# Performance work log

Hardware: AMD Instinct MI355X
Metric: run time of the kernel (lower is better)

The kernel has to match this reference:

```python
import jax, jax.numpy as jnp
import numpy as np


def setup_inputs() -> dict:
    key = jax.random.key(0)
    ks = jax.random.split(key, 8)
    B, S, H = 4, 2048, 1024
    heads = 16
    lim = 1.0 / np.sqrt(H)  # nn.Linear default init range
    x = jax.random.normal(ks[0], (B, S, H), dtype=jnp.float32)
    atten_mask = jnp.zeros((B, 1, S, 1), dtype=jnp.float32)  # 1.0 marks padded positions
    Wq = jax.random.uniform(ks[1], (H, H), jnp.float32, -lim, lim)
    bq = jax.random.uniform(ks[2], (H,), jnp.float32, -lim, lim)
    Wk = jax.random.uniform(ks[3], (H, H), jnp.float32, -lim, lim)
    bk = jax.random.uniform(ks[4], (H,), jnp.float32, -lim, lim)
    Wv = jax.random.uniform(ks[5], (H, H), jnp.float32, -lim, lim)
    bv = jax.random.uniform(ks[6], (H,), jnp.float32, -lim, lim)
    return {"x": x, "Wq": Wq, "bq": bq, "Wk": Wk, "bk": bk, "Wv": Wv, "bv": bv,
            "atten_mask": atten_mask, "attention_head_num": 16}


def reference(x, Wq, bq, Wk, bk, Wv, bv, atten_mask, attention_head_num):
    B, S, H = x.shape
    h = attention_head_num
    d = H // h
    # QKV projections (torch Linear: x @ W.T + b)
    q = (x @ Wq.T + bq).reshape(B, S, h, d).transpose(0, 2, 1, 3)  # [B,h,S,d]
    k = (x @ Wk.T + bk).reshape(B, S, h, d).transpose(0, 2, 1, 3)
    v = (x @ Wv.T + bv).reshape(B, S, h, d).transpose(0, 2, 1, 3)
    # combined padding + look-ahead mask: True -> masked
    causal = jnp.triu(jnp.ones((S, S), dtype=atten_mask.dtype), 1)  # [S,S]
    mask = (atten_mask + causal) >= 1.0  # [B,1 or h,S,S] broadcast
    mask = jnp.broadcast_to(mask, (B, h, S, S))
    scale = 1.0 / jnp.sqrt(jnp.asarray(d, dtype=jnp.float32))
    scores = jnp.einsum('bhqd,bhkd->bhqk', q, k) * scale
    scores = jnp.where(mask, jnp.float32(-1e9), scores)
    att = jax.nn.softmax(scores, axis=-1)
    out = jnp.einsum('bhqk,bhkd->bhqd', att, v)  # [B,h,S,d]
    return out.transpose(0, 2, 1, 3).reshape(B, S, H)
```

## Files before the change

kernel.cpp:

```cpp
#include <hip/hip_runtime.h>
#include <hip/hip_bf16.h>
#include <stdint.h>

typedef short v8s __attribute__((ext_vector_type(8)));
typedef float v4f __attribute__((ext_vector_type(4)));
typedef unsigned long long u64;
typedef unsigned short u16;
typedef unsigned int u32;
typedef u64 v2u __attribute__((ext_vector_type(2)));

__device__ __forceinline__ u16 f2bf(float f) {
    unsigned u = __builtin_bit_cast(unsigned, f);
    u += 0x7FFFu + ((u >> 16) & 1u);
    return (u16)(u >> 16);
}

__device__ __forceinline__ u32 cvt_pk_bf16(float lo, float hi) {
    u32 r;
    asm("v_cvt_pk_bf16_f32 %0, %1, %2" : "=v"(r) : "v"(lo), "v"(hi));
    return r;
}

__device__ __forceinline__ float ex2(float x) {
    float r;
    asm("v_exp_f32 %0, %1" : "=v"(r) : "v"(x));
    return r;
}

__device__ __forceinline__ void gload_lds16(const void* g, const void* lds) {
    __builtin_amdgcn_global_load_lds(
        (const __attribute__((address_space(1))) unsigned int*)(unsigned long long)g,
        (__attribute__((address_space(3))) unsigned int*)(unsigned int)(unsigned long long)lds,
        16, 0, 0);
}

__global__ __launch_bounds__(256) void cvt_all(const float* __restrict__ x,
                                               const float* __restrict__ wq,
                                               const float* __restrict__ wk,
                                               const float* __restrict__ wv,
                                               u16* __restrict__ xb, u16* __restrict__ wqb,
                                               u16* __restrict__ wkb, u16* __restrict__ wvb) {
    int i = blockIdx.x * 256 + threadIdx.x;
    const float* in;
    u16* out;
    if (i < 2097152)      { in = x;  out = xb; }
    else if (i < 2359296) { in = wq; out = wqb; i -= 2097152; }
    else if (i < 2621440) { in = wk; out = wkb; i -= 2359296; }
    else                  { in = wv; out = wvb; i -= 2621440; }
    float4 v = ((const float4*)in)[i];
    ((ushort4*)out)[i] = make_ushort4(f2bf(v.x), f2bf(v.y), f2bf(v.z), f2bf(v.w));
}

__global__ __launch_bounds__(256, 4)
void qkv_gemm_all(const u16* __restrict__ X,
                  const u16* __restrict__ Wq, const u16* __restrict__ Wk, const u16* __restrict__ Wv,
                  const float* __restrict__ bq, const float* __restrict__ bk, const float* __restrict__ bv,
                  u16* __restrict__ Qg, u16* __restrict__ Kg, u16* __restrict__ VTg) {
    __shared__ __align__(16) char smem[34816];
    char* ldsA = smem;
    char* ldsB = smem + 16384;
    u16*  ldsE = (u16*)smem;

    const int l = (blockIdx.x & 7) * 192 + (blockIdx.x >> 3);
    const int mode = l >> 9;
    const int bx = l & 511;
    const u16* W = (mode == 0) ? Wq : (mode == 1) ? Wk : Wv;
    const float* bias = (mode == 0) ? bq : (mode == 1) ? bk : bv;
    u16* Out = (mode == 0) ? Qg : (mode == 1) ? Kg : VTg;

    const int t = threadIdx.x;
    const int lane = t & 63, wave = t >> 6;
    const int lhi = lane >> 4, llo = lane & 15;
    const int wm = wave >> 1, wn = wave & 1;
    const int m0 = (bx >> 3) * 128;
    const int n0 = (bx & 7) * 128;

    const int srow = (t * 16) >> 7;
    const int ssc = ((t * 16) >> 4) & 7;
    v4f acc[4][4] = {};

    for (int k0 = 0; k0 < 1024; k0 += 64) {
        #pragma unroll
        for (int i = 0; i < 4; ++i) {
            int row = i * 32 + srow;
            int c = ssc ^ (row & 7);
            const char* wbaseA = ldsA + (i * 256 + wave * 64) * 16;
            const char* wbaseB = ldsB + (i * 256 + wave * 64) * 16;
            gload_lds16(X + (m0 + row) * 1024 + k0 + c * 8, wbaseA);
            gload_lds16(W + (n0 + row) * 1024 + k0 + c * 8, wbaseB);
        }
        __syncthreads();
        __builtin_amdgcn_s_setprio(1);
        #pragma unroll
        for (int s = 0; s < 2; ++s) {
            v8s af[4], bf[4];
            #pragma unroll
            for (int i = 0; i < 4; ++i) {
                int r = wm * 64 + i * 16 + llo;
                af[i] = *(const v8s*)(ldsA + r * 128 + (((lhi + 4 * s) ^ (r & 7)) << 4));
            }
            #pragma unroll
            for (int j = 0; j < 4; ++j) {
                int r = wn * 64 + j * 16 + llo;
                bf[j] = *(const v8s*)(ldsB + r * 128 + (((lhi + 4 * s) ^ (r & 7)) << 4));
            }
            #pragma unroll
            for (int i = 0; i < 4; ++i)
                #pragma unroll
                for (int j = 0; j < 4; ++j)
                    acc[i][j] = __builtin_amdgcn_mfma_f32_16x16x32_bf16(af[i], bf[j], acc[i][j], 0, 0, 0);
        }
        __builtin_amdgcn_s_setprio(0);
        __syncthreads();
    }

    float bv_[4];
    #pragma unroll
    for (int j = 0; j < 4; ++j) bv_[j] = bias[n0 + wn * 64 + j * 16 + llo];
    const float scl = (mode == 0) ? 0.18033688011112042f : 1.0f;

    #pragma unroll
    for (int i = 0; i < 4; ++i) {
        #pragma unroll
        for (int j = 0; j < 4; ++j) {
            #pragma unroll
            for (int r = 0; r < 4; ++r) {
                int ml = wm * 64 + i * 16 + lhi * 4 + r;
                int nl = wn * 64 + j * 16 + llo;
                float v = (acc[i][j][r] + bv_[j]) * scl;
                u16 hh = f2bf(v);
                if (mode == 2) ldsE[nl * 136 + ml] = hh;
                else           ldsE[ml * 136 + nl] = hh;
            }
        }
    }
    __syncthreads();

    const int row = t >> 1, half = t & 1;
    if (mode == 2) {
        int n = n0 + row, hh = n >> 6, dd = n & 63;
        int b = m0 >> 11, sbase = (m0 & 2047) + half * 64;
        u16* dst = Out + ((b * 16 + hh) * 64 + dd) * 2048 + sbase;
        #pragma unroll
        for (int j = 0; j < 8; ++j)
            *(v8s*)(dst + j * 8) = *(const v8s*)&ldsE[row * 136 + half * 64 + j * 8];
    } else {
        int m = m0 + row, b = m >> 11, s = m & 2047;
        int hh = (n0 + half * 64) >> 6;
        u16* dst = Out + ((b * 16 + hh) * 2048 + s) * 64;
        #pragma unroll
        for (int j = 0; j < 8; ++j)
            *(v8s*)(dst + j * 8) = *(const v8s*)&ldsE[row * 136 + half * 64 + j * 8];
    }
}

__global__ __launch_bounds__(256, 6)
void flash_attn(const u16* __restrict__ Qg, const u16* __restrict__ Kg,
                const u16* __restrict__ VTg, const float* __restrict__ am,
                float* __restrict__ out) {
    __shared__ __align__(16) char smem[25088];
    char* ldsK = smem;
    char* ldsV = smem + 8192;
    char* ldsP = smem + 16384 + (threadIdx.x >> 6) * 2176;

    const int t = threadIdx.x;
    const int lane = t & 63, wave = t >> 6;
    const int lhi = lane >> 4, llo = lane & 15;
    const int bh = blockIdx.x;
    const int qi = 31 - blockIdx.y;
    const int b = bh >> 4, h = bh & 15;
    const int qw = qi * 64 + wave * 16;
    const int q = qw + llo;

    v8s qf[2];
    #pragma unroll
    for (int s = 0; s < 2; ++s)
        qf[s] = *(const v8s*)(Qg + (bh * 2048 + q) * 64 + lhi * 8 + 32 * s);

    v8s ones;
    #pragma unroll
    for (int j = 0; j < 8; ++j) ones[j] = (short)0x3F80;

    const float rowpen = am[b * 2048 + q];

    const int srow = (t * 16) >> 7, ssc = ((t * 16) >> 4) & 7;
    const int sc1 = ssc ^ (srow & 7), sc2 = ssc ^ ((srow + 32) & 7);
    #define STAGE(kj2) do {                                                        \
        const int kv0_ = (kj2) * 64;                                               \
        const char* wbK = ldsK + (wave * 64) * 16;                                 \
        const char* wbV = ldsV + (wave * 64) * 16;                                 \
        gload_lds16(Kg + (bh * 2048 + kv0_ + srow) * 64 + sc1 * 8, wbK);           \
        gload_lds16(VTg + (bh * 64 + srow) * 2048 + kv0_ + sc1 * 8, wbV);          \
        gload_lds16(Kg + (bh * 2048 + kv0_ + srow + 32) * 64 + sc2 * 8, wbK + 4096); \
        gload_lds16(VTg + (bh * 64 + srow + 32) * 2048 + kv0_ + sc2 * 8, wbV + 4096); \
    } while (0)

    float mrow = -1e30f;
    v4f lsum_acc = {};
    v4f o_acc[4] = {};

    for (int kj = 0; kj <= qi; ++kj) {
        STAGE(kj);
        __syncthreads();
        const int kv0 = kj * 64;

        const int nt4 = (kj == qi) ? (wave + 1) : 4;
        v4f sacc[4] = {};
        __builtin_amdgcn_s_setprio(1);
        #pragma unroll
        for (int tt = 0; tt < 4; ++tt) {
            if (tt < nt4) {
                #pragma unroll
                for (int s = 0; s < 2; ++s) {
                    int row = tt * 16 + llo;
                    int c = lhi + 4 * s;
                    v8s kb = *(const v8s*)(ldsK + row * 128 + ((c ^ (row & 7)) << 4));
                    sacc[tt] = __builtin_amdgcn_mfma_f32_16x16x32_bf16(kb, qf[s], sacc[tt], 0, 0, 0);
                }
            }
        }
        __builtin_amdgcn_s_setprio(0);

        if (kj == qi) {
            #pragma unroll
            for (int tt = 0; tt < 4; ++tt)
                #pragma unroll
                for (int r = 0; r < 4; ++r) {
                    int kvg = kv0 + tt * 16 + lhi * 4 + r;
                    if (kvg > q) sacc[tt][r] = -1e30f;
                }
        }
        if (rowpen >= 1.0f) {
            #pragma unroll
            for (int tt = 0; tt < 4; ++tt)
                #pragma unroll
                for (int r = 0; r < 4; ++r) sacc[tt][r] = -1e30f;
        }

        float m0_ = fmaxf(fmaxf(sacc[0][0], sacc[0][1]), sacc[0][2]);
        float m1_ = fmaxf(fmaxf(sacc[0][3], sacc[1][0]), sacc[1][1]);
        float m2_ = fmaxf(fmaxf(sacc[1][2], sacc[1][3]), sacc[2][0]);
        float m3_ = fmaxf(fmaxf(sacc[2][1], sacc[2][2]), sacc[2][3]);
        float m4_ = fmaxf(fmaxf(sacc[3][0], sacc[3][1]), fmaxf(sacc[3][2], sacc[3][3]));
        float lmx = fmaxf(fmaxf(fmaxf(m0_, m1_), fmaxf(m2_, m3_)), m4_);

        if (__any(lmx > mrow + 8.0f)) {
            float mx = fmaxf(lmx, __shfl_xor(lmx, 16));
            mx = fmaxf(mx, __shfl_xor(mx, 32));
            const float mn = fmaxf(mrow, mx);
            const float sc_o = ex2(mrow - mn);
            mrow = mn;
            #pragma unroll
            for (int r = 0; r < 4; ++r) lsum_acc[r] *= sc_o;
            #pragma unroll
            for (int dt = 0; dt < 4; ++dt)
                #pragma unroll
                for (int r = 0; r < 4; ++r) o_acc[dt][r] *= sc_o;
        }

        #pragma unroll
        for (int tt = 0; tt < 4; ++tt) {
            float p0 = ex2(sacc[tt][0] - mrow);
            float p1 = ex2(sacc[tt][1] - mrow);
            float p2 = ex2(sacc[tt][2] - mrow);
            float p3 = ex2(sacc[tt][3] - mrow);
            u32 w0 = cvt_pk_bf16(p0, p1);
            u32 w1 = cvt_pk_bf16(p2, p3);
            *(u64*)(ldsP + llo * 136 + tt * 32 + lhi * 8) = (u64)w0 | ((u64)w1 << 32);
        }

        __builtin_amdgcn_s_setprio(1);
        #pragma unroll
        for (int s = 0; s < 2; ++s) {
            u64 plo = *(const u64*)(ldsP + llo * 136 + lhi * 16 + s * 64);
            u64 phi = *(const u64*)(ldsP + llo * 136 + lhi * 16 + s * 64 + 8);
            v2u tmp; tmp.x = plo; tmp.y = phi;
            v8s pb = __builtin_bit_cast(v8s, tmp);
            lsum_acc = __builtin_amdgcn_mfma_f32_16x16x32_bf16(ones, pb, lsum_acc, 0, 0, 0);
            #pragma unroll
            for (int dt = 0; dt < 4; ++dt) {
                int vrow = dt * 16 + llo;
                v8s vb = *(const v8s*)(ldsV + vrow * 128 + (((lhi + 4 * s) ^ (vrow & 7)) << 4));
                o_acc[dt] = __builtin_amdgcn_mfma_f32_16x16x32_bf16(vb, pb, o_acc[dt], 0, 0, 0);
            }
        }
        __builtin_amdgcn_s_setprio(0);
        __syncthreads();
    }

    const float inv = 1.0f / lsum_acc[0];
    float* dst = out + (size_t)(b * 2048 + q) * 1024 + h * 64 + lhi * 4;
    #pragma unroll
    for (int dt = 0; dt < 4; ++dt) {
        float4 o;
        o.x = o_acc[dt][0] * inv;
        o.y = o_acc[dt][1] * inv;
        o.z = o_acc[dt][2] * inv;
        o.w = o_acc[dt][3] * inv;
        *(float4*)(dst + dt * 16) = o;
    }
}

extern "C" void kernel_launch(void* const* d_in, const int* in_sizes, int n_in,
                              void* d_out, int out_size, void* d_ws, size_t ws_size,
                              hipStream_t stream) {
    const float* x  = (const float*)d_in[0];
    const float* Wq = (const float*)d_in[1];
    const float* bq = (const float*)d_in[2];
    const float* Wk = (const float*)d_in[3];
    const float* bk = (const float*)d_in[4];
    const float* Wv = (const float*)d_in[5];
    const float* bv = (const float*)d_in[6];
    const float* amask = (const float*)d_in[7];
    float* out = (float*)d_out;

    char* ws = (char*)d_ws;
    u16* xb  = (u16*)(ws);
    u16* Wqb = (u16*)(ws + 16777216);
    u16* Wkb = (u16*)(ws + 16777216 + 2097152);
    u16* Wvb = (u16*)(ws + 16777216 + 2 * 2097152);
    u16* Qg  = (u16*)(ws + 23068672);
    u16* Kg  = (u16*)(ws + 39845888);
    u16* VTg = (u16*)(ws + 56623104);

    cvt_all<<<11264, 256, 0, stream>>>(x, Wq, Wk, Wv, xb, Wqb, Wkb, Wvb);
    qkv_gemm_all<<<1536, 256, 0, stream>>>(xb, Wqb, Wkb, Wvb, bq, bk, bv, Qg, Kg, VTg);
    flash_attn<<<dim3(64, 32), 256, 0, stream>>>(Qg, Kg, VTg, amask, out);
}
```

Baseline: 148.7 us.

## Double-buffer LDS tiles in QKV GEMM with prefetch two stages ahead

Turns the QKV projection GEMM's single-buffered K loop into a two-stage LDS ping-pong. The next tile's global-to-LDS loads are issued while the current tile feeds the MFMAs, and explicit vmcnt waits plus raw barriers replace __syncthreads. This doubles LDS per block to 64KB and lowers the occupancy hint from 4 to 2 blocks per CU, trading latency hiding across waves for in-block overlap.

```diff
diff --git a/kernel.cpp b/kernel.cpp
--- a/kernel.cpp
+++ b/kernel.cpp
@@ -51,14 +51,14 @@
     ((ushort4*)out)[i] = make_ushort4(f2bf(v.x), f2bf(v.y), f2bf(v.z), f2bf(v.w));
 }
 
-__global__ __launch_bounds__(256, 4)
+__global__ __launch_bounds__(256, 2)
 void qkv_gemm_all(const u16* __restrict__ X,
                   const u16* __restrict__ Wq, const u16* __restrict__ Wk, const u16* __restrict__ Wv,
                   const float* __restrict__ bq, const float* __restrict__ bk, const float* __restrict__ bv,
                   u16* __restrict__ Qg, u16* __restrict__ Kg, u16* __restrict__ VTg) {
-    __shared__ __align__(16) char smem[34816];
+    __shared__ __align__(16) char smem[65536];
     char* ldsA = smem;
-    char* ldsB = smem + 16384;
+    char* ldsB = smem + 32768;
     u16*  ldsE = (u16*)smem;
 
     const int l = (blockIdx.x & 7) * 192 + (blockIdx.x >> 3);
@@ -79,17 +79,31 @@
     const int ssc = ((t * 16) >> 4) & 7;
     v4f acc[4][4] = {};
 
-    for (int k0 = 0; k0 < 1024; k0 += 64) {
-        #pragma unroll
-        for (int i = 0; i < 4; ++i) {
-            int row = i * 32 + srow;
-            int c = ssc ^ (row & 7);
-            const char* wbaseA = ldsA + (i * 256 + wave * 64) * 16;
-            const char* wbaseB = ldsB + (i * 256 + wave * 64) * 16;
-            gload_lds16(X + (m0 + row) * 1024 + k0 + c * 8, wbaseA);
-            gload_lds16(W + (n0 + row) * 1024 + k0 + c * 8, wbaseB);
-        }
-        __syncthreads();
+    #define GSTAGE(kt) do {                                                          \
+        const int k0_ = (kt) * 64;                                                   \
+        char* dA = ldsA + ((kt) & 1) * 16384;                                        \
+        char* dB = ldsB + ((kt) & 1) * 16384;                                        \
+        _Pragma("unroll")                                                            \
+        for (int i_ = 0; i_ < 4; ++i_) {                                             \
+            int row = i_ * 32 + srow;                                                \
+            int c = ssc ^ (row & 7);                     \
+            gload_lds16(X + (m0 + row) * 1024 + k0_ + c * 8,                         \
+                        dA + (i_ * 256 + wave * 64) * 16);                           \
+            gload_lds16(W + (n0 + row) * 1024 + k0_ + c * 8,                         \
+                        dB + (i_ * 256 + wave * 64) * 16);                           \
+        }                                                                            \
+    } while (0)
+
+    GSTAGE(0);
+    GSTAGE(1);
+
+    for (int kt = 0; kt < 16; ++kt) {
+        if (kt < 15) asm volatile("s_waitcnt vmcnt(8)" ::: "memory");
+        else         asm volatile("s_waitcnt vmcnt(0)" ::: "memory");
+        __builtin_amdgcn_s_barrier();
+
+        const char* cA = ldsA + (kt & 1) * 16384;
+        const char* cB = ldsB + (kt & 1) * 16384;
         __builtin_amdgcn_s_setprio(1);
         #pragma unroll
         for (int s = 0; s < 2; ++s) {
@@ -97,12 +111,12 @@
             #pragma unroll
             for (int i = 0; i < 4; ++i) {
                 int r = wm * 64 + i * 16 + llo;
-                af[i] = *(const v8s*)(ldsA + r * 128 + (((lhi + 4 * s) ^ (r & 7)) << 4));
+                af[i] = *(const v8s*)(cA + r * 128 + (((lhi + 4 * s) ^ (r & 7)) << 4));
             }
             #pragma unroll
             for (int j = 0; j < 4; ++j) {
                 int r = wn * 64 + j * 16 + llo;
-                bf[j] = *(const v8s*)(ldsB + r * 128 + (((lhi + 4 * s) ^ (r & 7)) << 4));
+                bf[j] = *(const v8s*)(cB + r * 128 + (((lhi + 4 * s) ^ (r & 7)) << 4));
             }
             #pragma unroll
             for (int i = 0; i < 4; ++i)
@@ -111,7 +125,8 @@
                     acc[i][j] = __builtin_amdgcn_mfma_f32_16x16x32_bf16(af[i], bf[j], acc[i][j], 0, 0, 0);
         }
         __builtin_amdgcn_s_setprio(0);
-        __syncthreads();
+        __builtin_amdgcn_s_barrier();
+        if (kt + 2 < 16) GSTAGE(kt + 2);
     }
 
     float bv_[4];
```

New measurement: 149.4 us. No clear change (+0.4%).

## Widen QKV GEMM block tile to 128x256 to raise operand reuse

Applied to the files above, without the earlier changes.

The QKV projection GEMM now uses 128x256 output tiles per block (each wave computes 64x128), halving the grid to 768 blocks and doubling per-block LDS for the B operand. The epilogue writes the two 128-column halves through LDS in two passes. This lowers global and LDS traffic per FLOP by reusing each A fragment across more MFMAs, at the cost of more accumulator registers, lower occupancy (launch bounds 2) and fewer blocks to spread over CUs.

```diff
diff --git a/kernel.cpp b/kernel.cpp
--- a/kernel.cpp
+++ b/kernel.cpp
@@ -51,19 +51,19 @@
     ((ushort4*)out)[i] = make_ushort4(f2bf(v.x), f2bf(v.y), f2bf(v.z), f2bf(v.w));
 }
 
-__global__ __launch_bounds__(256, 4)
+__global__ __launch_bounds__(256, 2)
 void qkv_gemm_all(const u16* __restrict__ X,
                   const u16* __restrict__ Wq, const u16* __restrict__ Wk, const u16* __restrict__ Wv,
                   const float* __restrict__ bq, const float* __restrict__ bk, const float* __restrict__ bv,
                   u16* __restrict__ Qg, u16* __restrict__ Kg, u16* __restrict__ VTg) {
-    __shared__ __align__(16) char smem[34816];
+    __shared__ __align__(16) char smem[49152];
     char* ldsA = smem;
     char* ldsB = smem + 16384;
     u16*  ldsE = (u16*)smem;
 
-    const int l = (blockIdx.x & 7) * 192 + (blockIdx.x >> 3);
-    const int mode = l >> 9;
-    const int bx = l & 511;
+    const int l = (blockIdx.x & 7) * 96 + (blockIdx.x >> 3);
+    const int mode = l >> 8;
+    const int bx = l & 255;
     const u16* W = (mode == 0) ? Wq : (mode == 1) ? Wk : Wv;
     const float* bias = (mode == 0) ? bq : (mode == 1) ? bk : bv;
     u16* Out = (mode == 0) ? Qg : (mode == 1) ? Kg : VTg;
@@ -72,85 +72,93 @@
     const int lane = t & 63, wave = t >> 6;
     const int lhi = lane >> 4, llo = lane & 15;
     const int wm = wave >> 1, wn = wave & 1;
-    const int m0 = (bx >> 3) * 128;
-    const int n0 = (bx & 7) * 128;
-
-    const int srow = (t * 16) >> 7;
-    const int ssc = ((t * 16) >> 4) & 7;
-    v4f acc[4][4] = {};
+    const int m0 = (bx >> 2) * 128;
+    const int n0 = (bx & 3) * 256;
+
+    const int srow = t >> 3;
+    const int ssc = t & 7;
+    v4f acc[4][8] = {};
 
     for (int k0 = 0; k0 < 1024; k0 += 64) {
         #pragma unroll
         for (int i = 0; i < 4; ++i) {
             int row = i * 32 + srow;
             int c = ssc ^ (row & 7);
-            const char* wbaseA = ldsA + (i * 256 + wave * 64) * 16;
-            const char* wbaseB = ldsB + (i * 256 + wave * 64) * 16;
-            gload_lds16(X + (m0 + row) * 1024 + k0 + c * 8, wbaseA);
-            gload_lds16(W + (n0 + row) * 1024 + k0 + c * 8, wbaseB);
+            gload_lds16(X + (m0 + row) * 1024 + k0 + c * 8,
+                        ldsA + (i * 256 + wave * 64) * 16);
+        }
+        #pragma unroll
+        for (int i = 0; i < 8; ++i) {
+            int row = i * 32 + srow;
+            int c = ssc ^ (row & 7);
+            gload_lds16(W + (n0 + row) * 1024 + k0 + c * 8,
+                        ldsB + (i * 256 + wave * 64) * 16);
         }
         __syncthreads();
         __builtin_amdgcn_s_setprio(1);
         #pragma unroll
         for (int s = 0; s < 2; ++s) {
-            v8s af[4], bf[4];
+            v8s af[4], bf[8];
             #pragma unroll
             for (int i = 0; i < 4; ++i) {
                 int r = wm * 64 + i * 16 + llo;
                 af[i] = *(const v8s*)(ldsA + r * 128 + (((lhi + 4 * s) ^ (r & 7)) << 4));
             }
             #pragma unroll
-            for (int j = 0; j < 4; ++j) {
-                int r = wn * 64 + j * 16 + llo;
+            for (int j = 0; j < 8; ++j) {
+                int r = wn * 128 + j * 16 + llo;
                 bf[j] = *(const v8s*)(ldsB + r * 128 + (((lhi + 4 * s) ^ (r & 7)) << 4));
             }
             #pragma unroll
             for (int i = 0; i < 4; ++i)
                 #pragma unroll
-                for (int j = 0; j < 4; ++j)
+                for (int j = 0; j < 8; ++j)
                     acc[i][j] = __builtin_amdgcn_mfma_f32_16x16x32_bf16(af[i], bf[j], acc[i][j], 0, 0, 0);
         }
         __builtin_amdgcn_s_setprio(0);
         __syncthreads();
     }
 
-    float bv_[4];
-    #pragma unroll
-    for (int j = 0; j < 4; ++j) bv_[j] = bias[n0 + wn * 64 + j * 16 + llo];
+    float bv_[8];
+    #pragma unroll
+    for (int j = 0; j < 8; ++j) bv_[j] = bias[n0 + wn * 128 + j * 16 + llo];
     const float scl = (mode == 0) ? 0.18033688011112042f : 1.0f;
 
     #pragma unroll
-    for (int i = 0; i < 4; ++i) {
-        #pragma unroll
-        for (int j = 0; j < 4; ++j) {
-            #pragma unroll
-            for (int r = 0; r < 4; ++r) {
-                int ml = wm * 64 + i * 16 + lhi * 4 + r;
-                int nl = wn * 64 + j * 16 + llo;
-                float v = (acc[i][j][r] + bv_[j]) * scl;
-                u16 hh = f2bf(v);
-                if (mode == 2) ldsE[nl * 136 + ml] = hh;
-                else           ldsE[ml * 136 + nl] = hh;
-            }
-        }
-    }
-    __syncthreads();
-
-    const int row = t >> 1, half = t & 1;
-    if (mode == 2) {
-        int n = n0 + row, hh = n >> 6, dd = n & 63;
-        int b = m0 >> 11, sbase = (m0 & 2047) + half * 64;
-        u16* dst = Out + ((b * 16 + hh) * 64 + dd) * 2048 + sbase;
-        #pragma unroll
-        for (int j = 0; j < 8; ++j)
-            *(v8s*)(dst + j * 8) = *(const v8s*)&ldsE[row * 136 + half * 64 + j * 8];
-    } else {
-        int m = m0 + row, b = m >> 11, s = m & 2047;
-        int hh = (n0 + half * 64) >> 6;
-        u16* dst = Out + ((b * 16 + hh) * 2048 + s) * 64;
-        #pragma unroll
-        for (int j = 0; j < 8; ++j)
-            *(v8s*)(dst + j * 8) = *(const v8s*)&ldsE[row * 136 + half * 64 + j * 8];
+    for (int hf = 0; hf < 2; ++hf) {
+        if (wn == hf) {
+            #pragma unroll
+            for (int i = 0; i < 4; ++i)
+                #pragma unroll
+                for (int j = 0; j < 8; ++j)
+                    #pragma unroll
+                    for (int r = 0; r < 4; ++r) {
+                        int ml = wm * 64 + i * 16 + lhi * 4 + r;
+                        int nl = j * 16 + llo;
+                        float v = (acc[i][j][r] + bv_[j]) * scl;
+                        u16 hb = f2bf(v);
+                        if (mode == 2) ldsE[nl * 136 + ml] = hb;
+                        else           ldsE[ml * 136 + nl] = hb;
+                    }
+        }
+        __syncthreads();
+        const int row = t >> 1, half = t & 1;
+        if (mode == 2) {
+            int n = n0 + hf * 128 + row, hh = n >> 6, dd = n & 63;
+            int b = m0 >> 11, sbase = (m0 & 2047) + half * 64;
+            u16* dst = Out + ((b * 16 + hh) * 64 + dd) * 2048 + sbase;
+            #pragma unroll
+            for (int j = 0; j < 8; ++j)
+                *(v8s*)(dst + j * 8) = *(const v8s*)&ldsE[row * 136 + half * 64 + j * 8];
+        } else {
+            int m = m0 + row, b = m >> 11, s2 = m & 2047;
+            int hh = (n0 + hf * 128 + half * 64) >> 6;
+            u16* dst = Out + ((b * 16 + hh) * 2048 + s2) * 64;
+            #pragma unroll
+            for (int j = 0; j < 8; ++j)
+                *(v8s*)(dst + j * 8) = *(const v8s*)&ldsE[row * 136 + half * 64 + j * 8];
+        }
+        __syncthreads();
     }
 }
 
@@ -324,6 +332,6 @@
     u16* VTg = (u16*)(ws + 56623104);
 
     cvt_all<<<11264, 256, 0, stream>>>(x, Wq, Wk, Wv, xb, Wqb, Wkb, Wvb);
-    qkv_gemm_all<<<1536, 256, 0, stream>>>(xb, Wqb, Wkb, Wvb, bq, bk, bv, Qg, Kg, VTg);
+    qkv_gemm_all<<<768, 256, 0, stream>>>(xb, Wqb, Wkb, Wvb, bq, bk, bv, Qg, Kg, VTg);
     flash_attn<<<dim3(64, 32), 256, 0, stream>>>(Qg, Kg, VTg, amask, out);
 }
```

Result: slower. 155.5 us (+4.5%).

## Process two 64-row query tiles per flash-attention block to reuse staged K/V

Applied to the files above, without the earlier changes.

Each flash-attention block now handles 128 query rows, as two 64-row tiles A and B, instead of 64. Every K/V tile loaded into LDS is consumed by both query tiles, which halves global-to-LDS traffic and the number of barriers per unit of work. The grid shrinks to 16 blocks in y and the launch bound drops to 4 waves per EU to accommodate the doubled accumulators. The cost is higher register pressure, fewer resident blocks, coarser causal load balance, and one extra KV tile per block processed only for tile B.

```diff
diff --git a/kernel.cpp b/kernel.cpp
--- a/kernel.cpp
+++ b/kernel.cpp
@@ -154,7 +154,7 @@
     }
 }
 
-__global__ __launch_bounds__(256, 6)
+__global__ __launch_bounds__(256, 4)
 void flash_attn(const u16* __restrict__ Qg, const u16* __restrict__ Kg,
                 const u16* __restrict__ VTg, const float* __restrict__ am,
                 float* __restrict__ out) {
@@ -167,21 +167,25 @@
     const int lane = t & 63, wave = t >> 6;
     const int lhi = lane >> 4, llo = lane & 15;
     const int bh = blockIdx.x;
-    const int qi = 31 - blockIdx.y;
+    const int qi = 15 - blockIdx.y;
     const int b = bh >> 4, h = bh & 15;
-    const int qw = qi * 64 + wave * 16;
-    const int q = qw + llo;
-
-    v8s qf[2];
+    const int qwA = qi * 128 + wave * 16;
+    const int qA = qwA + llo;
+    const int qB = qA + 64;
+
+    v8s qfA[2], qfB[2];
     #pragma unroll
-    for (int s = 0; s < 2; ++s)
-        qf[s] = *(const v8s*)(Qg + (bh * 2048 + q) * 64 + lhi * 8 + 32 * s);
+    for (int s = 0; s < 2; ++s) {
+        qfA[s] = *(const v8s*)(Qg + (bh * 2048 + qA) * 64 + lhi * 8 + 32 * s);
+        qfB[s] = *(const v8s*)(Qg + (bh * 2048 + qB) * 64 + lhi * 8 + 32 * s);
+    }
 
     v8s ones;
     #pragma unroll
     for (int j = 0; j < 8; ++j) ones[j] = (short)0x3F80;
 
-    const float rowpen = am[b * 2048 + q];
+    const float rowpenA = am[b * 2048 + qA];
+    const float rowpenB = am[b * 2048 + qB];
 
     const int srow = (t * 16) >> 7, ssc = ((t * 16) >> 4) & 7;
     const int sc1 = ssc ^ (srow & 7), sc2 = ssc ^ ((srow + 32) & 7);
@@ -195,109 +199,204 @@
         gload_lds16(VTg + (bh * 64 + srow + 32) * 2048 + kv0_ + sc2 * 8, wbV + 4096); \
     } while (0)
 
-    float mrow = -1e30f;
-    v4f lsum_acc = {};
-    v4f o_acc[4] = {};
-
-    for (int kj = 0; kj <= qi; ++kj) {
+    float mrowA = -1e30f, mrowB = -1e30f;
+    v4f lsumA = {}, lsumB = {};
+    v4f oA[4] = {}, oB[4] = {};
+
+    const int ntiles = 2 * qi + 2;
+    for (int kj = 0; kj < ntiles; ++kj) {
         STAGE(kj);
         __syncthreads();
         const int kv0 = kj * 64;
 
-        const int nt4 = (kj == qi) ? (wave + 1) : 4;
-        v4f sacc[4] = {};
-        __builtin_amdgcn_s_setprio(1);
-        #pragma unroll
-        for (int tt = 0; tt < 4; ++tt) {
-            if (tt < nt4) {
-                #pragma unroll
-                for (int s = 0; s < 2; ++s) {
-                    int row = tt * 16 + llo;
-                    int c = lhi + 4 * s;
-                    v8s kb = *(const v8s*)(ldsK + row * 128 + ((c ^ (row & 7)) << 4));
-                    sacc[tt] = __builtin_amdgcn_mfma_f32_16x16x32_bf16(kb, qf[s], sacc[tt], 0, 0, 0);
+        if (kj <= 2 * qi) {
+            const int ntA = (kj == 2 * qi) ? (wave + 1) : 4;
+            v4f sacc[4] = {};
+            __builtin_amdgcn_s_setprio(1);
+            #pragma unroll
+            for (int tt = 0; tt < 4; ++tt) {
+                if (tt < ntA) {
+                    #pragma unroll
+                    for (int s = 0; s < 2; ++s) {
+                        int row = tt * 16 + llo;
+                        int c = lhi + 4 * s;
+                        v8s kb = *(const v8s*)(ldsK + row * 128 + ((c ^ (row & 7)) << 4));
+                        sacc[tt] = __builtin_amdgcn_mfma_f32_16x16x32_bf16(kb, qfA[s], sacc[tt], 0, 0, 0);
+                    }
                 }
             }
+            __builtin_amdgcn_s_setprio(0);
+
+            if (kj == 2 * qi) {
+                #pragma unroll
+                for (int tt = 0; tt < 4; ++tt)
+                    #pragma unroll
+                    for (int r = 0; r < 4; ++r) {
+                        int kvg = kv0 + tt * 16 + lhi * 4 + r;
+                        if (kvg > qA) sacc[tt][r] = -1e30f;
+                    }
+            }
+            if (rowpenA >= 1.0f) {
+                #pragma unroll
+                for (int tt = 0; tt < 4; ++tt)
+                    #pragma unroll
+                    for (int r = 0; r < 4; ++r) sacc[tt][r] = -1e30f;
+            }
+
+            float m0_ = fmaxf(fmaxf(sacc[0][0], sacc[0][1]), sacc[0][2]);
+            float m1_ = fmaxf(fmaxf(sacc[0][3], sacc[1][0]), sacc[1][1]);
+            float m2_ = fmaxf(fmaxf(sacc[1][2], sacc[1][3]), sacc[2][0]);
+            float m3_ = fmaxf(fmaxf(sacc[2][1], sacc[2][2]), sacc[2][3]);
+            float m4_ = fmaxf(fmaxf(sacc[3][0], sacc[3][1]), fmaxf(sacc[3][2], sacc[3][3]));
+            float lmx = fmaxf(fmaxf(fmaxf(m0_, m1_), fmaxf(m2_, m3_)), m4_);
+
+            if (__any(lmx > mrowA + 8.0f)) {
+                float mx = fmaxf(lmx, __shfl_xor(lmx, 16));
+                mx = fmaxf(mx, __shfl_xor(mx, 32));
+                const float mn = fmaxf(mrowA, mx);
+                const float sc_o = ex2(mrowA - mn);
+                mrowA = mn;
+                #pragma unroll
+                for (int r = 0; r < 4; ++r) lsumA[r] *= sc_o;
+                #pragma unroll
+                for (int dt = 0; dt < 4; ++dt)
+                    #pragma unroll
+                    for (int r = 0; r < 4; ++r) oA[dt][r] *= sc_o;
+            }
+
+            #pragma unroll
+            for (int tt = 0; tt < 4; ++tt) {
+                float p0 = ex2(sacc[tt][0] - mrowA);
+                float p1 = ex2(sacc[tt][1] - mrowA);
+                float p2 = ex2(sacc[tt][2] - mrowA);
+                float p3 = ex2(sacc[tt][3] - mrowA);
+                u32 w0 = cvt_pk_bf16(p0, p1);
+                u32 w1 = cvt_pk_bf16(p2, p3);
+                *(u64*)(ldsP + llo * 136 + tt * 32 + lhi * 8) = (u64)w0 | ((u64)w1 << 32);
+            }
+
+            __builtin_amdgcn_s_setprio(1);
+            #pragma unroll
+            for (int s = 0; s < 2; ++s) {
+                u64 plo = *(const u64*)(ldsP + llo * 136 + lhi * 16 + s * 64);
+                u64 phi = *(const u64*)(ldsP + llo * 136 + lhi * 16 + s * 64 + 8);
+                v2u tmp; tmp.x = plo; tmp.y = phi;
+                v8s pb = __builtin_bit_cast(v8s, tmp);
+                lsumA = __builtin_amdgcn_mfma_f32_16x16x32_bf16(ones, pb, lsumA, 0, 0, 0);
+                #pragma unroll
+                for (int dt = 0; dt < 4; ++dt) {
+                    int vrow = dt * 16 + llo;
+                    v8s vb = *(const v8s*)(ldsV + vrow * 128 + (((lhi + 4 * s) ^ (vrow & 7)) << 4));
+                    oA[dt] = __builtin_amdgcn_mfma_f32_16x16x32_bf16(vb, pb, oA[dt], 0, 0, 0);
+                }
+            }
+            __builtin_amdgcn_s_setprio(0);
         }
-        __builtin_amdgcn_s_setprio(0);
-
-        if (kj == qi) {
-            #pragma unroll
-            for (int tt = 0; tt < 4; ++tt)
-                #pragma unroll
-                for (int r = 0; r < 4; ++r) {
-                    int kvg = kv0 + tt * 16 + lhi * 4 + r;
-                    if (kvg > q) sacc[tt][r] = -1e30f;
+
+        {
+            const int ntB = (kj == 2 * qi + 1) ? (wave + 1) : 4;
+            v4f sacc[4] = {};
+            __builtin_amdgcn_s_setprio(1);
+            #pragma unroll
+            for (int tt = 0; tt < 4; ++tt) {
+                if (tt < ntB) {
+                    #pragma unroll
+                    for (int s = 0; s < 2; ++s) {
+                        int row = tt * 16 + llo;
+                        int c = lhi + 4 * s;
+                        v8s kb = *(const v8s*)(ldsK + row * 128 + ((c ^ (row & 7)) << 4));
+                        sacc[tt] = __builtin_amdgcn_mfma_f32_16x16x32_bf16(kb, qfB[s], sacc[tt], 0, 0, 0);
+                    }
                 }
+            }
+            __builtin_amdgcn_s_setprio(0);
+
+            if (kj == 2 * qi + 1) {
+                #pragma unroll
+                for (int tt = 0; tt < 4; ++tt)
+                    #pragma unroll
+                    for (int r = 0; r < 4; ++r) {
+                        int kvg = kv0 + tt * 16 + lhi * 4 + r;
+                        if (kvg > qB) sacc[tt][r] = -1e30f;
+                    }
+            }
+            if (rowpenB >= 1.0f) {
+                #pragma unroll
+                for (int tt = 0; tt < 4; ++tt)
+                    #pragma unroll
+                    for (int r = 0; r < 4; ++r) sacc[tt][r] = -1e30f;
+            }
+
+            float m0_ = fmaxf(fmaxf(sacc[0][0], sacc[0][1]), sacc[0][2]);
+            float m1_ = fmaxf(fmaxf(sacc[0][3], sacc[1][0]), sacc[1][1]);
+            float m2_ = fmaxf(fmaxf(sacc[1][2], sacc[1][3]), sacc[2][0]);
+            float m3_ = fmaxf(fmaxf(sacc[2][1], sacc[2][2]), sacc[2][3]);
+            float m4_ = fmaxf(fmaxf(sacc[3][0], sacc[3][1]), fmaxf(sacc[3][2], sacc[3][3]));
+            float lmx = fmaxf(fmaxf(fmaxf(m0_, m1_), fmaxf(m2_, m3_)), m4_);
+
+            if (__any(lmx > mrowB + 8.0f)) {
+                float mx = fmaxf(lmx, __shfl_xor(lmx, 16));
+                mx = fmaxf(mx, __shfl_xor(mx, 32));
+                const float mn = fmaxf(mrowB, mx);
+                const float sc_o = ex2(mrowB - mn);
+                mrowB = mn;
+                #pragma unroll
+                for (int r = 0; r < 4; ++r) lsumB[r] *= sc_o;
+                #pragma unroll
+                for (int dt = 0; dt < 4; ++dt)
+                    #pragma unroll
+                    for (int r = 0; r < 4; ++r) oB[dt][r] *= sc_o;
+            }
+
+            #pragma unroll
+            for (int tt = 0; tt < 4; ++tt) {
+                float p0 = ex2(sacc[tt][0] - mrowB);
+                float p1 = ex2(sacc[tt][1] - mrowB);
+                float p2 = ex2(sacc[tt][2] - mrowB);
+                float p3 = ex2(sacc[tt][3] - mrowB);
+                u32 w0 = cvt_pk_bf16(p0, p1);
+                u32 w1 = cvt_pk_bf16(p2, p3);
+                *(u64*)(ldsP + llo * 136 + tt * 32 + lhi * 8) = (u64)w0 | ((u64)w1 << 32);
+            }
+
+            __builtin_amdgcn_s_setprio(1);
+            #pragma unroll
+            for (int s = 0; s < 2; ++s) {
+                u64 plo = *(const u64*)(ldsP + llo * 136 + lhi * 16 + s * 64);
+                u64 phi = *(const u64*)(ldsP + llo * 136 + lhi * 16 + s * 64 + 8);
+                v2u tmp; tmp.x = plo; tmp.y = phi;
+                v8s pb = __builtin_bit_cast(v8s, tmp);
+                lsumB = __builtin_amdgcn_mfma_f32_16x16x32_bf16(ones, pb, lsumB, 0, 0, 0);
+                #pragma unroll
+                for (int dt = 0; dt < 4; ++dt) {
+                    int vrow = dt * 16 + llo;
+                    v8s vb = *(const v8s*)(ldsV + vrow * 128 + (((lhi + 4 * s) ^ (vrow & 7)) << 4));
+                    oB[dt] = __builtin_amdgcn_mfma_f32_16x16x32_bf16(vb, pb, oB[dt], 0, 0, 0);
+                }
+            }
+            __builtin_amdgcn_s_setprio(0);
         }
-        if (rowpen >= 1.0f) {
-            #pragma unroll
-            for (int tt = 0; tt < 4; ++tt)
-                #pragma unroll
-                for (int r = 0; r < 4; ++r) sacc[tt][r] = -1e30f;
-        }
-
-        float m0_ = fmaxf(fmaxf(sacc[0][0], sacc[0][1]), sacc[0][2]);
-        float m1_ = fmaxf(fmaxf(sacc[0][3], sacc[1][0]), sacc[1][1]);
-        float m2_ = fmaxf(fmaxf(sacc[1][2], sacc[1][3]), sacc[2][0]);
-        float m3_ = fmaxf(fmaxf(sacc[2][1], sacc[2][2]), sacc[2][3]);
-        float m4_ = fmaxf(fmaxf(sacc[3][0], sacc[3][1]), fmaxf(sacc[3][2], sacc[3][3]));
-        float lmx = fmaxf(fmaxf(fmaxf(m0_, m1_), fmaxf(m2_, m3_)), m4_);
-
-        if (__any(lmx > mrow + 8.0f)) {
-            float mx = fmaxf(lmx, __shfl_xor(lmx, 16));
-            mx = fmaxf(mx, __shfl_xor(mx, 32));
-            const float mn = fmaxf(mrow, mx);
-            const float sc_o = ex2(mrow - mn);
-            mrow = mn;
-            #pragma unroll
-            for (int r = 0; r < 4; ++r) lsum_acc[r] *= sc_o;
-            #pragma unroll
-            for (int dt = 0; dt < 4; ++dt)
-                #pragma unroll
-                for (int r = 0; r < 4; ++r) o_acc[dt][r] *= sc_o;
-        }
-
-        #pragma unroll
-        for (int tt = 0; tt < 4; ++tt) {
-            float p0 = ex2(sacc[tt][0] - mrow);
-            float p1 = ex2(sacc[tt][1] - mrow);
-            float p2 = ex2(sacc[tt][2] - mrow);
-            float p3 = ex2(sacc[tt][3] - mrow);
-            u32 w0 = cvt_pk_bf16(p0, p1);
-            u32 w1 = cvt_pk_bf16(p2, p3);
-            *(u64*)(ldsP + llo * 136 + tt * 32 + lhi * 8) = (u64)w0 | ((u64)w1 << 32);
-        }
-
-        __builtin_amdgcn_s_setprio(1);
-        #pragma unroll
-        for (int s = 0; s < 2; ++s) {
-            u64 plo = *(const u64*)(ldsP + llo * 136 + lhi * 16 + s * 64);
-            u64 phi = *(const u64*)(ldsP + llo * 136 + lhi * 16 + s * 64 + 8);
-            v2u tmp; tmp.x = plo; tmp.y = phi;
-            v8s pb = __builtin_bit_cast(v8s, tmp);
-            lsum_acc = __builtin_amdgcn_mfma_f32_16x16x32_bf16(ones, pb, lsum_acc, 0, 0, 0);
-            #pragma unroll
-            for (int dt = 0; dt < 4; ++dt) {
-                int vrow = dt * 16 + llo;
-                v8s vb = *(const v8s*)(ldsV + vrow * 128 + (((lhi + 4 * s) ^ (vrow & 7)) << 4));
-                o_acc[dt] = __builtin_amdgcn_mfma_f32_16x16x32_bf16(vb, pb, o_acc[dt], 0, 0, 0);
-            }
-        }
-        __builtin_amdgcn_s_setprio(0);
         __syncthreads();
     }
 
-    const float inv = 1.0f / lsum_acc[0];
-    float* dst = out + (size_t)(b * 2048 + q) * 1024 + h * 64 + lhi * 4;
+    const float invA = 1.0f / lsumA[0];
+    const float invB = 1.0f / lsumB[0];
+    float* dstA = out + (size_t)(b * 2048 + qA) * 1024 + h * 64 + lhi * 4;
+    float* dstB = out + (size_t)(b * 2048 + qB) * 1024 + h * 64 + lhi * 4;
     #pragma unroll
     for (int dt = 0; dt < 4; ++dt) {
         float4 o;
-        o.x = o_acc[dt][0] * inv;
-        o.y = o_acc[dt][1] * inv;
-        o.z = o_acc[dt][2] * inv;
-        o.w = o_acc[dt][3] * inv;
-        *(float4*)(dst + dt * 16) = o;
+        o.x = oA[dt][0] * invA;
+        o.y = oA[dt][1] * invA;
+        o.z = oA[dt][2] * invA;
+        o.w = oA[dt][3] * invA;
+        *(float4*)(dstA + dt * 16) = o;
+        float4 p;
+        p.x = oB[dt][0] * invB;
+        p.y = oB[dt][1] * invB;
+        p.z = oB[dt][2] * invB;
+        p.w = oB[dt][3] * invB;
+        *(float4*)(dstB + dt * 16) = p;
     }
 }
 
@@ -325,5 +424,5 @@
 
     cvt_all<<<11264, 256, 0, stream>>>(x, Wq, Wk, Wv, xb, Wqb, Wkb, Wvb);
     qkv_gemm_all<<<1536, 256, 0, stream>>>(xb, Wqb, Wkb, Wvb, bq, bk, bv, Qg, Kg, VTg);
-    flash_attn<<<dim3(64, 32), 256, 0, stream>>>(Qg, Kg, VTg, amask, out);
-}
+    flash_attn<<<dim3(64, 16), 256, 0, stream>>>(Qg, Kg, VTg, amask, out);
+}
```

Result: slower. 155.7 us (+4.7%).
